# Kernel tuning notes

Hardware: AMD Instinct MI355X
Metric: run time of the kernel (lower is better)

## Reference

```python
import jax, jax.numpy as jnp
import numpy as np

B, D_IN, H1, H2, LAT, K = 32768, 512, 256, 128, 64, 2048
BN_EPS = 1e-5
COMMIT = 0.25


def _linear_w(k, i, o):
    # xavier-uniform-ish init
    lim = np.sqrt(6.0 / (i + o)).astype(np.float32)
    return jax.random.uniform(k, (i, o), jnp.float32, -lim, lim)


def _bn_params(keys, n):
    g = jax.random.uniform(keys[0], (n,), jnp.float32, 0.5, 1.5)
    b = 0.1 * jax.random.normal(keys[1], (n,), jnp.float32)
    m = 0.1 * jax.random.normal(keys[2], (n,), jnp.float32)
    v = jax.random.uniform(keys[3], (n,), jnp.float32, 0.5, 1.5)
    return g, b, m, v


def setup_inputs() -> dict:
    key = jax.random.key(0)
    ks = jax.random.split(key, 32)
    inp = {"x": jax.random.normal(ks[0], (B, D_IN), jnp.float32)}
    # encoder: 512 -> 256 -> 128 -> 64
    inp["ew1"], inp["eb1"] = _linear_w(ks[1], D_IN, H1), jnp.zeros((H1,), jnp.float32)
    inp["eg1"], inp["ebt1"], inp["em1"], inp["ev1"] = _bn_params(jax.random.split(ks[2], 4), H1)
    inp["ew2"], inp["eb2"] = _linear_w(ks[3], H1, H2), jnp.zeros((H2,), jnp.float32)
    inp["eg2"], inp["ebt2"], inp["em2"], inp["ev2"] = _bn_params(jax.random.split(ks[4], 4), H2)
    inp["ew3"], inp["eb3"] = _linear_w(ks[5], H2, LAT), jnp.zeros((LAT,), jnp.float32)
    # codebook (num_embeddings, latent_dim)
    inp["codebook"] = _linear_w(ks[6], K, LAT).reshape(K, LAT)
    # decoder: 64 -> 128 -> 256 -> 512
    inp["dw1"], inp["db1"] = _linear_w(ks[7], LAT, H2), jnp.zeros((H2,), jnp.float32)
    inp["dg1"], inp["dbt1"], inp["dm1"], inp["dv1"] = _bn_params(jax.random.split(ks[8], 4), H2)
    inp["dw2"], inp["db2"] = _linear_w(ks[9], H2, H1), jnp.zeros((H1,), jnp.float32)
    inp["dg2"], inp["dbt2"], inp["dm2"], inp["dv2"] = _bn_params(jax.random.split(ks[10], 4), H1)
    inp["dw3"], inp["db3"] = _linear_w(ks[11], H1, D_IN), jnp.zeros((D_IN,), jnp.float32)
    return inp


def _bn(x, g, b, m, v):
    # BatchNorm1d in eval mode: running stats
    return (x - m) * (g * jax.lax.rsqrt(v + BN_EPS)) + b


def reference(x, ew1, eb1, eg1, ebt1, em1, ev1,
              ew2, eb2, eg2, ebt2, em2, ev2,
              ew3, eb3, codebook,
              dw1, db1, dg1, dbt1, dm1, dv1,
              dw2, db2, dg2, dbt2, dm2, dv2,
              dw3, db3):
    # ---- encoder MLP (Dropout is identity in eval) ----
    h = _bn(jax.nn.relu(x @ ew1 + eb1), eg1, ebt1, em1, ev1)
    h = _bn(jax.nn.relu(h @ ew2 + eb2), eg2, ebt2, em2, ev2)
    z_e = h @ ew3 + eb3  # [B, LAT]

    # ---- vector quantization: cdist + argmin + gather ----
    # squared L2 distance (argmin-equivalent to cdist p=2)
    d2 = (jnp.sum(z_e * z_e, axis=1, keepdims=True)
          + jnp.sum(codebook * codebook, axis=1)[None, :]
          - 2.0 * (z_e @ codebook.T))  # [B, K]
    idx = jnp.argmin(d2, axis=-1)  # [B]
    z_q = codebook[idx]  # gather, [B, LAT]

    codebook_loss = jnp.mean((z_q - jax.lax.stop_gradient(z_e)) ** 2)
    commit_loss = jnp.mean((z_e - jax.lax.stop_gradient(z_q)) ** 2)
    vq_loss = codebook_loss + COMMIT * commit_loss

    # straight-through estimator
    z_q = z_e + jax.lax.stop_gradient(z_q - z_e)

    # ---- decoder MLP ----
    h = _bn(jax.nn.relu(z_q @ dw1 + db1), dg1, dbt1, dm1, dv1)
    h = _bn(jax.nn.relu(h @ dw2 + db2), dg2, dbt2, dm2, dv2)
    x_recon = h @ dw3 + db3  # [B, D_IN]

    recon_err = jnp.mean((x_recon - x) ** 2)
    return x_recon, vq_loss, idx, recon_err
```

## Files before the change

### kernel.cpp

```cpp
#include <hip/hip_runtime.h>

#define B_ROWS 32768
#define D_IN   512
#define H1_N   256
#define H2_N   128
#define LAT_N  64
#define K_CB   2048

#define VQ_MARGIN 6.0e-3f
#define BK 32
#define BN 128

typedef __attribute__((ext_vector_type(8))) short s8v;
typedef __attribute__((ext_vector_type(4))) float f4v;

__device__ inline unsigned short f2bf(float f) {
    union { float f; unsigned u; } v; v.f = f;
    unsigned r = v.u + 0x7fffu + ((v.u >> 16) & 1u);
    return (unsigned short)(r >> 16);
}
__device__ inline float bf2f(unsigned short h) {
    union { unsigned u; float f; } v; v.u = ((unsigned)h) << 16;
    return v.f;
}

__device__ inline int pidx(int r, int k, int K) {
    return ((r >> 4) * (K >> 5) + (k >> 5)) * 512 + (((k >> 3) & 3) << 7)
         + ((r & 15) << 3) + (k & 7);
}

#define SWZ(row) ((((row) >> 2) & 7) << 3)

__global__ __launch_bounds__(256) void xsplit(
    const float* __restrict__ x, unsigned short* __restrict__ xhi,
    unsigned short* __restrict__ xlo)
{
    int t = blockIdx.x * 256 + threadIdx.x;
    int r = t >> 6;
    int g = t & 63;
    const float* p = &x[(size_t)r * D_IN + g * 8];
    float4 v0 = *reinterpret_cast<const float4*>(p);
    float4 v1 = *reinterpret_cast<const float4*>(p + 4);
    float fv[8] = {v0.x, v0.y, v0.z, v0.w, v1.x, v1.y, v1.z, v1.w};
    union { unsigned short s[8]; uint4 v; } H, L;
#pragma unroll
    for (int j = 0; j < 8; ++j) {
        unsigned u = __float_as_uint(fv[j]);
        float lo = fv[j] - __uint_as_float(u & 0xffff0000u);
        H.s[j] = (unsigned short)(u >> 16);
        L.s[j] = f2bf(lo);
    }
    int pp = pidx(r, g * 8, D_IN);
    *reinterpret_cast<uint4*>(&xhi[pp]) = H.v;
    *reinterpret_cast<uint4*>(&xlo[pp]) = L.v;
}

template <int MODE, int K, int CT>
__global__ __launch_bounds__(256, 2) void mfma_gemm(
    const unsigned short* __restrict__ A_hi,
    const unsigned short* __restrict__ A_lo,
    const unsigned short* __restrict__ w_hi,
    const unsigned short* __restrict__ w_lo,
    const float* __restrict__ bias,
    const float* __restrict__ bn_g, const float* __restrict__ bn_b,
    const float* __restrict__ bn_m, const float* __restrict__ bn_v,
    unsigned short* __restrict__ out_hi, unsigned short* __restrict__ out_lo,
    float* __restrict__ out_f32,
    const float* __restrict__ xref, float* __restrict__ partials, int N)
{
    constexpr int NK = K / 32;
    const int lane = threadIdx.x & 63;
    const int wv = threadIdx.x >> 6;
    const int wr = wv >> 1, wc = wv & 1;
    const int rbase = blockIdx.x * 128 + wr * 64;
    const int cbase = blockIdx.y * (32 * CT) + wc * (16 * CT);
    const int lr = lane & 15, lg = lane >> 4;
    const int lofs = lg * 128 + lr * 8;

    f4v acc[4][CT];
#pragma unroll
    for (int rt = 0; rt < 4; ++rt)
#pragma unroll
        for (int ct = 0; ct < CT; ++ct)
            acc[rt][ct] = (f4v){0.f, 0.f, 0.f, 0.f};

    s8v ahA[4], alA[4], bhA[CT], blA[CT];
    s8v ahB[4], alB[4], bhB[CT], blB[CT];

#define LOADF(S, KS)                                                          \
    {                                                                         \
        _Pragma("unroll")                                                     \
        for (int rt = 0; rt < 4; ++rt) {                                      \
            int aoff = (((rbase >> 4) + rt) * NK + (KS)) * 512 + lofs;        \
            ah##S[rt] = *reinterpret_cast<const s8v*>(&A_hi[aoff]);           \
            al##S[rt] = *reinterpret_cast<const s8v*>(&A_lo[aoff]);           \
        }                                                                     \
        _Pragma("unroll")                                                     \
        for (int ct = 0; ct < CT; ++ct) {                                     \
            int woff = (((cbase >> 4) + ct) * NK + (KS)) * 512 + lofs;        \
            bh##S[ct] = *reinterpret_cast<const s8v*>(&w_hi[woff]);           \
            bl##S[ct] = *reinterpret_cast<const s8v*>(&w_lo[woff]);           \
        }                                                                     \
    }

#define MFMAF(S)                                                              \
    {                                                                         \
        _Pragma("unroll")                                                     \
        for (int rt = 0; rt < 4; ++rt)                                        \
            _Pragma("unroll")                                                 \
            for (int ct = 0; ct < CT; ++ct) {                                 \
                acc[rt][ct] = __builtin_amdgcn_mfma_f32_16x16x32_bf16(        \
                    ah##S[rt], bh##S[ct], acc[rt][ct], 0, 0, 0);              \
                acc[rt][ct] = __builtin_amdgcn_mfma_f32_16x16x32_bf16(        \
                    al##S[rt], bh##S[ct], acc[rt][ct], 0, 0, 0);              \
                acc[rt][ct] = __builtin_amdgcn_mfma_f32_16x16x32_bf16(        \
                    ah##S[rt], bl##S[ct], acc[rt][ct], 0, 0, 0);              \
            }                                                                 \
    }

    LOADF(A, 0);
#pragma unroll
    for (int k2 = 0; k2 < NK / 2; ++k2) {
        LOADF(B, 2 * k2 + 1);
        MFMAF(A);
        if (k2 + 1 < NK / 2) LOADF(A, 2 * k2 + 2);
        MFMAF(B);
    }
#undef LOADF
#undef MFMAF

    float sq = 0.f;
#pragma unroll
    for (int ct = 0; ct < CT; ++ct) {
        int col = cbase + ct * 16 + lr;
        float bi = bias[col];
        float sc = 0.f, sh = 0.f;
        if (MODE == 0) {
            float s = bn_g[col] * rsqrtf(bn_v[col] + 1e-5f);
            sc = s;
            sh = bn_b[col] - bn_m[col] * s;
        }
#pragma unroll
        for (int rt = 0; rt < 4; ++rt)
#pragma unroll
            for (int i = 0; i < 4; ++i) {
                int row = rbase + rt * 16 + lg * 4 + i;
                float v = acc[rt][ct][i] + bi;
                if (MODE == 0) v = fmaxf(v, 0.f) * sc + sh;
                if (MODE == 0 || MODE == 3) {
                    unsigned u = __float_as_uint(v);
                    int p = pidx(row, col, N);
                    out_hi[p] = (unsigned short)(u >> 16);
                    out_lo[p] = f2bf(v - __uint_as_float(u & 0xffff0000u));
                }
                if (MODE == 2) {
                    float d = v - xref[(size_t)row * N + col];
                    sq = fmaf(d, d, sq);
                }
                if (MODE == 2 || MODE == 3)
                    out_f32[(size_t)row * N + col] = v;
            }
    }
    if (MODE == 2) {
        __shared__ float red[256];
        red[threadIdx.x] = sq;
        __syncthreads();
        for (int off = 128; off > 0; off >>= 1) {
            if (threadIdx.x < off) red[threadIdx.x] += red[threadIdx.x + off];
            __syncthreads();
        }
        if (threadIdx.x == 0)
            partials[blockIdx.y * gridDim.x + blockIdx.x] = red[0];
    }
}

template <int MODE, bool GATHER>
__global__ __launch_bounds__(256, 6) void rgemm(
    const int* __restrict__ rcnt, const int* __restrict__ rlist,
    const float* __restrict__ A, const float* __restrict__ W,
    const float* __restrict__ bias,
    const float* __restrict__ bn_g, const float* __restrict__ bn_b,
    const float* __restrict__ bn_m, const float* __restrict__ bn_v,
    float* __restrict__ out, int M, int N)
{
    const int count = min(rcnt[0], B_ROWS);
    const int row0 = blockIdx.x * 64;
    if (row0 >= count) return;
    __shared__ float sA[BK][64];
    __shared__ float sB[BK][BN];
    const int tid = threadIdx.x;
    const int tr = tid >> 4;
    const int tc = tid & 15;
    const int n0 = blockIdx.y * BN;

    float acc[4][8];
#pragma unroll
    for (int i = 0; i < 4; ++i)
#pragma unroll
        for (int j = 0; j < 8; ++j) acc[i][j] = 0.f;

    for (int k0 = 0; k0 < M; k0 += BK) {
#pragma unroll
        for (int it = 0; it < 2; ++it) {
            int s = tid + it * 256;
            int m = s >> 3;
            int kq = s & 7;
            int i = row0 + m;
            int src;
            if (GATHER) {
                int rr = (i < count) ? rlist[i] : 0;
                src = ((unsigned)rr < (unsigned)B_ROWS) ? rr : 0;
            } else {
                src = i;
            }
            float4 v = *reinterpret_cast<const float4*>(
                &A[(size_t)src * M + k0 + kq * 4]);
            int kk = kq * 4;
            sA[kk + 0][m ^ SWZ(kk + 0)] = v.x;
            sA[kk + 1][m ^ SWZ(kk + 1)] = v.y;
            sA[kk + 2][m ^ SWZ(kk + 2)] = v.z;
            sA[kk + 3][m ^ SWZ(kk + 3)] = v.w;
        }
#pragma unroll
        for (int it = 0; it < 4; ++it) {
            int s = tid + it * 256;
            int k = s >> 5;
            int nq = s & 31;
            int n = n0 + nq * 4;
            float4 v = make_float4(0.f, 0.f, 0.f, 0.f);
            if (n < N)
                v = *reinterpret_cast<const float4*>(&W[(size_t)(k0 + k) * N + n]);
            *reinterpret_cast<float4*>(&sB[k][nq * 4]) = v;
        }
        __syncthreads();
#pragma unroll 4
        for (int k = 0; k < BK; ++k) {
            int ac = (tr * 4) ^ SWZ(k);
            float4 a0 = *reinterpret_cast<float4*>(&sA[k][ac]);
            float a[4] = {a0.x, a0.y, a0.z, a0.w};
            float4 b0 = *reinterpret_cast<float4*>(&sB[k][tc * 4]);
            float4 b1 = *reinterpret_cast<float4*>(&sB[k][64 + tc * 4]);
            float b[8] = {b0.x, b0.y, b0.z, b0.w, b1.x, b1.y, b1.z, b1.w};
#pragma unroll
            for (int i = 0; i < 4; ++i)
#pragma unroll
                for (int j = 0; j < 8; ++j)
                    acc[i][j] = fmaf(a[i], b[j], acc[i][j]);
        }
        __syncthreads();
    }

    const int nb0 = n0 + tc * 4;
    const int nb1 = n0 + 64 + tc * 4;
    float bi[8], sc[8], sh[8];
#pragma unroll
    for (int g = 0; g < 2; ++g) {
        int nb = g ? nb1 : nb0;
        if (nb < N) {
#pragma unroll
            for (int j = 0; j < 4; ++j) {
                int n = nb + j;
                bi[g * 4 + j] = bias[n];
                if (MODE == 0) {
                    float s = bn_g[n] * rsqrtf(bn_v[n] + 1e-5f);
                    sc[g * 4 + j] = s;
                    sh[g * 4 + j] = bn_b[n] - bn_m[n] * s;
                }
            }
        }
    }
#pragma unroll
    for (int i = 0; i < 4; ++i) {
        int row = row0 + tr * 4 + i;
#pragma unroll
        for (int g = 0; g < 2; ++g) {
            int nb = g ? nb1 : nb0;
            if (nb < N) {
                float o[4];
#pragma unroll
                for (int j = 0; j < 4; ++j) {
                    float v = acc[i][g * 4 + j] + bi[g * 4 + j];
                    if (MODE == 0) {
                        v = v > 0.f ? v : 0.f;
                        v = v * sc[g * 4 + j] + sh[g * 4 + j];
                    }
                    o[j] = v;
                }
                *reinterpret_cast<float4*>(&out[(size_t)row * N + nb]) =
                    make_float4(o[0], o[1], o[2], o[3]);
            }
        }
    }
}

__device__ inline void wprep_packed(const float* __restrict__ w,
                                    unsigned short* __restrict__ w_hi,
                                    unsigned short* __restrict__ w_lo,
                                    int K, int N, int t)
{
    if (t >= N * (K >> 3)) return;
    int n = t / (K >> 3);
    int k0 = (t - n * (K >> 3)) << 3;
    union { unsigned short s[8]; uint4 v; } H, L;
#pragma unroll
    for (int j = 0; j < 8; ++j) {
        float f = w[(size_t)(k0 + j) * N + n];
        unsigned u = __float_as_uint(f);
        float lo = f - __uint_as_float(u & 0xffff0000u);
        H.s[j] = (unsigned short)(u >> 16);
        L.s[j] = f2bf(lo);
    }
    int p = pidx(n, k0, K);
    *reinterpret_cast<uint4*>(&w_hi[p]) = H.v;
    *reinterpret_cast<uint4*>(&w_lo[p]) = L.v;
}

__global__ __launch_bounds__(256) void prep_all(
    const float* __restrict__ dw3, unsigned short* w3hi, unsigned short* w3lo,
    const float* __restrict__ dw2, unsigned short* w2hi, unsigned short* w2lo,
    const float* __restrict__ dw1, unsigned short* w1hi, unsigned short* w1lo,
    const float* __restrict__ ew1, unsigned short* e1hi, unsigned short* e1lo,
    const float* __restrict__ ew2, unsigned short* e2hi, unsigned short* e2lo,
    const float* __restrict__ ew3, unsigned short* e3hi, unsigned short* e3lo,
    const float* __restrict__ cb, unsigned short* cb_hi, unsigned short* cb_lo,
    float* __restrict__ cn, int* __restrict__ rcnt, float* __restrict__ repairp)
{
    int bid = blockIdx.x;
    int tid = threadIdx.x;
    if (bid < 64) {
        wprep_packed(dw3, w3hi, w3lo, H1_N, D_IN, bid * 256 + tid);
    } else if (bid < 80) {
        wprep_packed(dw2, w2hi, w2lo, H2_N, H1_N, (bid - 64) * 256 + tid);
    } else if (bid < 84) {
        wprep_packed(dw1, w1hi, w1lo, LAT_N, H2_N, (bid - 80) * 256 + tid);
    } else if (bid < 148) {
        wprep_packed(ew1, e1hi, e1lo, D_IN, H1_N, (bid - 84) * 256 + tid);
    } else if (bid < 164) {
        wprep_packed(ew2, e2hi, e2lo, H1_N, H2_N, (bid - 148) * 256 + tid);
    } else if (bid < 168) {
        wprep_packed(ew3, e3hi, e3lo, H2_N, LAT_N, (bid - 164) * 256 + tid);
    } else {
        int blk = bid - 168;
        if (blk == 0) {
            if (tid == 0) rcnt[0] = 0;
            repairp[tid] = 0.f;
        }
        int j = blk * 256 + tid;
        float s = 0.f;
#pragma unroll
        for (int g = 0; g < 8; ++g) {
            float4 v0 = *reinterpret_cast<const float4*>(&cb[(size_t)j * LAT_N + g * 8]);
            float4 v1 = *reinterpret_cast<const float4*>(&cb[(size_t)j * LAT_N + g * 8 + 4]);
            float e[8] = {v0.x, v0.y, v0.z, v0.w, v1.x, v1.y, v1.z, v1.w};
            union { unsigned short us[8]; uint4 v; } H, L;
#pragma unroll
            for (int t = 0; t < 8; ++t) {
                s = fmaf(e[t], e[t], s);
                unsigned short hb = f2bf(e[t]);
                H.us[t] = hb;
                L.us[t] = f2bf(e[t] - bf2f(hb));
            }
            int p = pidx(j, g * 8, LAT_N);
            *reinterpret_cast<uint4*>(&cb_hi[p]) = H.v;
            *reinterpret_cast<uint4*>(&cb_lo[p]) = L.v;
        }
        cn[j] = s;
    }
}

__global__ __launch_bounds__(256) void vq_mfma(
    const unsigned short* __restrict__ zhi, const unsigned short* __restrict__ zlo,
    const unsigned short* __restrict__ cb_hi,
    const unsigned short* __restrict__ cb_lo, const float* __restrict__ cnorm,
    float4* __restrict__ cand)
{
    const int lane = threadIdx.x & 63;
    const int wid  = blockIdx.x * 4 + (threadIdx.x >> 6);
    const int rbase = (wid >> 3) * 64;
    const int cblk  = wid & 7;
    const int cbase = cblk * 256;
    const int lr = lane & 15;
    const int lg = lane >> 4;

    s8v a_hi[4][2], a_lo[4][2];
#pragma unroll
    for (int rt = 0; rt < 4; ++rt) {
#pragma unroll
        for (int ks = 0; ks < 2; ++ks) {
            int off = (((rbase >> 4) + rt) * 2 + ks) * 512 + lg * 128 + lr * 8;
            a_hi[rt][ks] = *reinterpret_cast<const s8v*>(&zhi[off]);
            a_lo[rt][ks] = *reinterpret_cast<const s8v*>(&zlo[off]);
        }
    }

    float b1[4][4], b2[4][4];
    int j1[4][4];
#pragma unroll
    for (int rt = 0; rt < 4; ++rt)
#pragma unroll
        for (int i = 0; i < 4; ++i) {
            b1[rt][i] = 3.4e38f; b2[rt][i] = 3.4e38f; j1[rt][i] = 0;
        }

    for (int ct = 0; ct < 16; ++ct) {
        int col = cbase + ct * 16 + lr;
        int t0 = (((cbase >> 4) + ct) * 2 + 0) * 512 + lg * 128 + lr * 8;
        int t1 = t0 + 512;
        s8v bh0 = *reinterpret_cast<const s8v*>(&cb_hi[t0]);
        s8v bh1 = *reinterpret_cast<const s8v*>(&cb_hi[t1]);
        s8v bl0 = *reinterpret_cast<const s8v*>(&cb_lo[t0]);
        s8v bl1 = *reinterpret_cast<const s8v*>(&cb_lo[t1]);
        float cn = cnorm[col];
#pragma unroll
        for (int rt = 0; rt < 4; ++rt) {
            f4v acc = {0.f, 0.f, 0.f, 0.f};
            acc = __builtin_amdgcn_mfma_f32_16x16x32_bf16(a_hi[rt][0], bh0, acc, 0, 0, 0);
            acc = __builtin_amdgcn_mfma_f32_16x16x32_bf16(a_hi[rt][1], bh1, acc, 0, 0, 0);
            acc = __builtin_amdgcn_mfma_f32_16x16x32_bf16(a_lo[rt][0], bh0, acc, 0, 0, 0);
            acc = __builtin_amdgcn_mfma_f32_16x16x32_bf16(a_lo[rt][1], bh1, acc, 0, 0, 0);
            acc = __builtin_amdgcn_mfma_f32_16x16x32_bf16(a_hi[rt][0], bl0, acc, 0, 0, 0);
            acc = __builtin_amdgcn_mfma_f32_16x16x32_bf16(a_hi[rt][1], bl1, acc, 0, 0, 0);
#pragma unroll
            for (int i = 0; i < 4; ++i) {
                float d = fmaf(-2.f, acc[i], cn);
                if (d < b1[rt][i]) {
                    b2[rt][i] = b1[rt][i];
                    b1[rt][i] = d;
                    j1[rt][i] = col;
                } else if (d < b2[rt][i]) {
                    b2[rt][i] = d;
                }
            }
        }
    }

#pragma unroll
    for (int off = 1; off < 16; off <<= 1) {
#pragma unroll
        for (int rt = 0; rt < 4; ++rt)
#pragma unroll
            for (int i = 0; i < 4; ++i) {
                float o1 = __shfl_xor(b1[rt][i], off);
                float o2 = __shfl_xor(b2[rt][i], off);
                int oj = __shfl_xor(j1[rt][i], off);
                float nb2 = fminf(fmaxf(b1[rt][i], o1), fminf(b2[rt][i], o2));
                if (o1 < b1[rt][i] ||
                    (o1 == b1[rt][i] && oj < j1[rt][i])) {
                    b1[rt][i] = o1;
                    j1[rt][i] = oj;
                }
                b2[rt][i] = nb2;
            }
    }
    if (lr == 0) {
#pragma unroll
        for (int rt = 0; rt < 4; ++rt)
#pragma unroll
            for (int i = 0; i < 4; ++i) {
                int row = rbase + rt * 16 + lg * 4 + i;
                cand[(size_t)row * 8 + cblk] = make_float4(
                    b1[rt][i], __int_as_float(j1[rt][i]), b2[rt][i], 0.f);
            }
    }
}

__global__ __launch_bounds__(256) void vq_merge(
    const float4* __restrict__ cand, const float* __restrict__ z,
    const float* __restrict__ cb,
    const unsigned short* __restrict__ cbhi,
    const unsigned short* __restrict__ cblo,
    unsigned short* __restrict__ zqhi, unsigned short* __restrict__ zqlo,
    float* __restrict__ idxf,
    int* __restrict__ rlist, int* __restrict__ rcnt,
    float* __restrict__ mergep)
{
    __shared__ float red[256];
    int tid = threadIdx.x;
    int row = blockIdx.x * 256 + tid;
    const float4* c = &cand[(size_t)row * 8];
    float4 c0 = c[0];
    float b1 = c0.x, b2 = c0.z;
    int j1 = __float_as_int(c0.y);
#pragma unroll
    for (int t = 1; t < 8; ++t) {
        float4 ct = c[t];
        float o1 = ct.x, o2 = ct.z;
        int oj = __float_as_int(ct.y);
        float nb2 = fminf(fmaxf(b1, o1), fminf(b2, o2));
        if (o1 < b1 || (o1 == b1 && oj < j1)) { b1 = o1; j1 = oj; }
        b2 = nb2;
    }
    idxf[row] = (float)j1;
    float sq = 0.f;
    if (b2 - b1 >= VQ_MARGIN) {
#pragma unroll
        for (int lq = 0; lq < 16; ++lq) {
            float4 cv = *reinterpret_cast<const float4*>(&cb[(size_t)j1 * LAT_N + lq * 4]);
            float4 zv = *reinterpret_cast<const float4*>(&z[(size_t)row * LAT_N + lq * 4]);
            float d0 = cv.x - zv.x, d1 = cv.y - zv.y;
            float d2 = cv.z - zv.z, d3 = cv.w - zv.w;
            sq = fmaf(d0, d0, sq); sq = fmaf(d1, d1, sq);
            sq = fmaf(d2, d2, sq); sq = fmaf(d3, d3, sq);
        }
#pragma unroll
        for (int g = 0; g < 8; ++g) {
            int sp = pidx(j1, g * 8, LAT_N);
            int dp = pidx(row, g * 8, LAT_N);
            *reinterpret_cast<uint4*>(&zqhi[dp]) =
                *reinterpret_cast<const uint4*>(&cbhi[sp]);
            *reinterpret_cast<uint4*>(&zqlo[dp]) =
                *reinterpret_cast<const uint4*>(&cblo[sp]);
        }
    } else {
        int s = atomicAdd(rcnt, 1);
        if (s < B_ROWS) rlist[s] = row;
    }
    red[tid] = sq;
    __syncthreads();
    for (int off = 128; off > 0; off >>= 1) {
        if (tid < off) red[tid] += red[tid + off];
        __syncthreads();
    }
    if (tid == 0) mergep[blockIdx.x] = red[0];
}

#define RB 8
__global__ __launch_bounds__(256) void repair_scan(
    const int* __restrict__ rcnt, const int* __restrict__ rlist,
    const float* __restrict__ zr,
    const float* __restrict__ cb, const float* __restrict__ cn,
    const unsigned short* __restrict__ cbhi,
    const unsigned short* __restrict__ cblo,
    unsigned short* __restrict__ zqhi, unsigned short* __restrict__ zqlo,
    float* __restrict__ idxf, float* __restrict__ repairp)
{
    __shared__ float sz[RB][LAT_N];
    __shared__ float rv[256];
    __shared__ int ri[256];
    const int tid = threadIdx.x;
    const int count = min(rcnt[0], B_ROWS);
    if (blockIdx.x * RB >= count) return;
    float lsum = 0.f;
    for (int base = blockIdx.x * RB; base < count; base += gridDim.x * RB) {
        int nr = min(RB, count - base);
        __syncthreads();
        for (int s = tid; s < nr * LAT_N; s += 256) {
            int r = s >> 6, d = s & 63;
            sz[r][d] = zr[(size_t)(base + r) * LAT_N + d];
        }
        __syncthreads();
        float bv[RB];
        int bj[RB];
#pragma unroll
        for (int r = 0; r < RB; ++r) { bv[r] = 3.4e38f; bj[r] = 0; }
        for (int k = 0; k < K_CB / 256; ++k) {
            int cidx = tid + k * 256;
            float a[RB];
#pragma unroll
            for (int r = 0; r < RB; ++r) a[r] = 0.f;
            const float* cp = &cb[(size_t)cidx * LAT_N];
#pragma unroll 2
            for (int d4 = 0; d4 < 16; ++d4) {
                float4 cv = *reinterpret_cast<const float4*>(cp + d4 * 4);
#pragma unroll
                for (int r = 0; r < RB; ++r) {
                    a[r] = fmaf(sz[r][d4 * 4 + 0], cv.x, a[r]);
                    a[r] = fmaf(sz[r][d4 * 4 + 1], cv.y, a[r]);
                    a[r] = fmaf(sz[r][d4 * 4 + 2], cv.z, a[r]);
                    a[r] = fmaf(sz[r][d4 * 4 + 3], cv.w, a[r]);
                }
            }
            float cnv = cn[cidx];
#pragma unroll
            for (int r = 0; r < RB; ++r) {
                float d = fmaf(-2.f, a[r], cnv);
                if (d < bv[r] || (d == bv[r] && cidx < bj[r])) {
                    bv[r] = d; bj[r] = cidx;
                }
            }
        }
        for (int r = 0; r < RB; ++r) {
            if (r >= nr) break;
            rv[tid] = bv[r];
            ri[tid] = bj[r];
            __syncthreads();
            for (int off = 128; off > 0; off >>= 1) {
                if (tid < off) {
                    float ov = rv[tid + off];
                    int oi = ri[tid + off];
                    if (ov < rv[tid] || (ov == rv[tid] && oi < ri[tid])) {
                        rv[tid] = ov; ri[tid] = oi;
                    }
                }
                __syncthreads();
            }
            int bjf = ri[0];
            int rr = rlist[base + r];
            bool ok = (unsigned)rr < (unsigned)B_ROWS;
            rr = ok ? rr : 0;
            if (tid == 0 && ok) idxf[rr] = (float)bjf;
            float v = 0.f;
            if (tid < 64) {
                float d = cb[(size_t)bjf * LAT_N + tid] - sz[r][tid];
                v = d * d;
            }
            __syncthreads();
            rv[tid] = v;
            __syncthreads();
            for (int off = 128; off > 0; off >>= 1) {
                if (tid < off) rv[tid] += rv[tid + off];
                __syncthreads();
            }
            if (tid == 0) lsum += rv[0];
            if (ok) {
                if (tid < 8) {
                    int g = tid;
                    *reinterpret_cast<uint4*>(&zqhi[pidx(rr, g * 8, LAT_N)]) =
                        *reinterpret_cast<const uint4*>(&cbhi[pidx(bjf, g * 8, LAT_N)]);
                } else if (tid < 16) {
                    int g = tid - 8;
                    *reinterpret_cast<uint4*>(&zqlo[pidx(rr, g * 8, LAT_N)]) =
                        *reinterpret_cast<const uint4*>(&cblo[pidx(bjf, g * 8, LAT_N)]);
                }
            }
            __syncthreads();
        }
    }
    if (tid == 0) repairp[blockIdx.x] = lsum;
}

__global__ __launch_bounds__(256) void finalize_kernel(
    const float* __restrict__ mergep, int nm,
    const float* __restrict__ repairp, int nr,
    const float* __restrict__ rep, int nre,
    float* __restrict__ vq_out, float* __restrict__ re_out)
{
    __shared__ float s[256];
    int tid = threadIdx.x;
    float a = 0.f;
    for (int i = tid; i < nm; i += 256) a += mergep[i];
    for (int i = tid; i < nr; i += 256) a += repairp[i];
    s[tid] = a;
    __syncthreads();
    for (int off = 128; off > 0; off >>= 1) {
        if (tid < off) s[tid] += s[tid + off];
        __syncthreads();
    }
    if (tid == 0) *vq_out = 1.25f * s[0] / (float)(B_ROWS * LAT_N);
    __syncthreads();
    float b = 0.f;
    for (int i = tid; i < nre; i += 256) b += rep[i];
    s[tid] = b;
    __syncthreads();
    for (int off = 128; off > 0; off >>= 1) {
        if (tid < off) s[tid] += s[tid + off];
        __syncthreads();
    }
    if (tid == 0) *re_out = s[0] / (float)(B_ROWS * D_IN);
}

extern "C" void kernel_launch(void* const* d_in, const int* in_sizes, int n_in,
                              void* d_out, int out_size, void* d_ws, size_t ws_size,
                              hipStream_t stream)
{
    const float* x    = (const float*)d_in[0];
    const float* ew1  = (const float*)d_in[1];
    const float* eb1  = (const float*)d_in[2];
    const float* eg1  = (const float*)d_in[3];
    const float* ebt1 = (const float*)d_in[4];
    const float* em1  = (const float*)d_in[5];
    const float* ev1  = (const float*)d_in[6];
    const float* ew2  = (const float*)d_in[7];
    const float* eb2  = (const float*)d_in[8];
    const float* eg2  = (const float*)d_in[9];
    const float* ebt2 = (const float*)d_in[10];
    const float* em2  = (const float*)d_in[11];
    const float* ev2  = (const float*)d_in[12];
    const float* ew3  = (const float*)d_in[13];
    const float* eb3  = (const float*)d_in[14];
    const float* cb   = (const float*)d_in[15];
    const float* dw1  = (const float*)d_in[16];
    const float* db1  = (const float*)d_in[17];
    const float* dg1  = (const float*)d_in[18];
    const float* dbt1 = (const float*)d_in[19];
    const float* dm1  = (const float*)d_in[20];
    const float* dv1  = (const float*)d_in[21];
    const float* dw2  = (const float*)d_in[22];
    const float* db2  = (const float*)d_in[23];
    const float* dg2  = (const float*)d_in[24];
    const float* dbt2 = (const float*)d_in[25];
    const float* dm2  = (const float*)d_in[26];
    const float* dv2  = (const float*)d_in[27];
    const float* dw3  = (const float*)d_in[28];
    const float* db3  = (const float*)d_in[29];

    float* outf = (float*)d_out;
    const size_t XR_OFF = 0;
    const size_t VQ_OFF = (size_t)B_ROWS * D_IN;
    const size_t IDX_OFF = VQ_OFF + 1;
    const size_t RE_OFF = IDX_OFF + B_ROWS;

    float* wsf = (float*)d_ws;
    size_t off = 0;
    float* buf256 = wsf + off; off += (size_t)B_ROWS * H1_N;
    float* buf128 = wsf + off; off += (size_t)B_ROWS * H2_N;
    float* zbuf   = wsf + off; off += (size_t)B_ROWS * LAT_N;
    float* zr     = wsf + off; off += (size_t)B_ROWS * LAT_N;
    float* cnbuf  = wsf + off; off += K_CB;
    float* mergep = wsf + off; off += 128;
    float* repairp= wsf + off; off += 256;
    float* rep    = wsf + off; off += 1024;
    unsigned short* cbhi = (unsigned short*)(wsf + off); off += K_CB * LAT_N / 2;
    unsigned short* cblo = (unsigned short*)(wsf + off); off += K_CB * LAT_N / 2;
    float4* candb = (float4*)(wsf + off); off += (size_t)B_ROWS * 8 * 4;
    int* rcnt  = (int*)(wsf + off); off += 16;
    int* rlist = (int*)(wsf + off); off += B_ROWS;
    unsigned short* w1hi = (unsigned short*)(wsf + off); off += (H2_N * LAT_N) / 2;
    unsigned short* w1lo = (unsigned short*)(wsf + off); off += (H2_N * LAT_N) / 2;
    unsigned short* w2hi = (unsigned short*)(wsf + off); off += (H1_N * H2_N) / 2;
    unsigned short* w2lo = (unsigned short*)(wsf + off); off += (H1_N * H2_N) / 2;
    unsigned short* w3hi = (unsigned short*)(wsf + off); off += (D_IN * H1_N) / 2;
    unsigned short* w3lo = (unsigned short*)(wsf + off); off += (D_IN * H1_N) / 2;
    unsigned short* e1hi = (unsigned short*)(wsf + off); off += (D_IN * H1_N) / 2;
    unsigned short* e1lo = (unsigned short*)(wsf + off); off += (D_IN * H1_N) / 2;
    unsigned short* e2hi = (unsigned short*)(wsf + off); off += (H1_N * H2_N) / 2;
    unsigned short* e2lo = (unsigned short*)(wsf + off); off += (H1_N * H2_N) / 2;
    unsigned short* e3hi = (unsigned short*)(wsf + off); off += (H2_N * LAT_N) / 2;
    unsigned short* e3lo = (unsigned short*)(wsf + off); off += (H2_N * LAT_N) / 2;
    unsigned short* zqhi = (unsigned short*)(wsf + off); off += (size_t)B_ROWS * LAT_N / 2;
    unsigned short* zqlo = (unsigned short*)(wsf + off); off += (size_t)B_ROWS * LAT_N / 2;
    unsigned short* xhi  = (unsigned short*)(wsf + off); off += (size_t)B_ROWS * D_IN / 2;
    unsigned short* xlo  = (unsigned short*)(wsf + off); off += (size_t)B_ROWS * D_IN / 2;

    unsigned short* eh1hi = (unsigned short*)buf256;
    unsigned short* eh1lo = (unsigned short*)(buf256 + (size_t)B_ROWS * 128);
    unsigned short* zhi   = (unsigned short*)buf256;
    unsigned short* zlo   = (unsigned short*)(buf256 + (size_t)B_ROWS * 32);
    float*          h1r   = buf256;
    unsigned short* dh2hi = (unsigned short*)buf256;
    unsigned short* dh2lo = (unsigned short*)(buf256 + (size_t)B_ROWS * 128);
    unsigned short* eh2hi = (unsigned short*)buf128;
    unsigned short* eh2lo = (unsigned short*)(buf128 + (size_t)B_ROWS * 64);
    float*          h2r   = buf128;
    unsigned short* dh1hi = (unsigned short*)buf128;
    unsigned short* dh1lo = (unsigned short*)(buf128 + (size_t)B_ROWS * 64);

    dim3 blk(256);
    const int GXM = B_ROWS / 128;
    const int GM64 = B_ROWS / 64;

    prep_all<<<dim3(176), blk, 0, stream>>>(
        dw3, w3hi, w3lo, dw2, w2hi, w2lo, dw1, w1hi, w1lo,
        ew1, e1hi, e1lo, ew2, e2hi, e2lo, ew3, e3hi, e3lo,
        cb, cbhi, cblo, cnbuf, rcnt, repairp);
    xsplit<<<dim3(B_ROWS * (D_IN / 8) / 256), blk, 0, stream>>>(x, xhi, xlo);

    mfma_gemm<0, D_IN, 4><<<dim3(GXM, H1_N / 128), blk, 0, stream>>>(
        xhi, xlo, e1hi, e1lo, eb1, eg1, ebt1, em1, ev1,
        eh1hi, eh1lo, nullptr, nullptr, nullptr, H1_N);
    mfma_gemm<0, H1_N, 4><<<dim3(GXM, 1), blk, 0, stream>>>(
        eh1hi, eh1lo, e2hi, e2lo, eb2, eg2, ebt2, em2, ev2,
        eh2hi, eh2lo, nullptr, nullptr, nullptr, H2_N);
    mfma_gemm<3, H2_N, 2><<<dim3(GXM, 1), blk, 0, stream>>>(
        eh2hi, eh2lo, e3hi, e3lo, eb3, nullptr, nullptr, nullptr, nullptr,
        zhi, zlo, zbuf, nullptr, nullptr, LAT_N);

    vq_mfma<<<dim3(1024), blk, 0, stream>>>(zhi, zlo, cbhi, cblo, cnbuf, candb);
    vq_merge<<<dim3(B_ROWS / 256), blk, 0, stream>>>(
        candb, zbuf, cb, cbhi, cblo, zqhi, zqlo,
        outf + IDX_OFF, rlist, rcnt, mergep);

    rgemm<0, true><<<dim3(GM64, 2), blk, 0, stream>>>(
        rcnt, rlist, x, ew1, eb1, eg1, ebt1, em1, ev1, h1r, D_IN, H1_N);
    rgemm<0, false><<<dim3(GM64, 1), blk, 0, stream>>>(
        rcnt, rlist, h1r, ew2, eb2, eg2, ebt2, em2, ev2, h2r, H1_N, H2_N);
    rgemm<1, false><<<dim3(GM64, 1), blk, 0, stream>>>(
        rcnt, rlist, h2r, ew3, eb3, nullptr, nullptr, nullptr, nullptr,
        zr, H2_N, LAT_N);
    repair_scan<<<dim3(256), blk, 0, stream>>>(
        rcnt, rlist, zr, cb, cnbuf, cbhi, cblo, zqhi, zqlo,
        outf + IDX_OFF, repairp);

    mfma_gemm<0, LAT_N, 4><<<dim3(GXM, 1), blk, 0, stream>>>(
        zqhi, zqlo, w1hi, w1lo, db1, dg1, dbt1, dm1, dv1,
        dh1hi, dh1lo, nullptr, nullptr, nullptr, H2_N);
    mfma_gemm<0, H2_N, 4><<<dim3(GXM, H1_N / 128), blk, 0, stream>>>(
        dh1hi, dh1lo, w2hi, w2lo, db2, dg2, dbt2, dm2, dv2,
        dh2hi, dh2lo, nullptr, nullptr, nullptr, H1_N);
    mfma_gemm<2, H1_N, 4><<<dim3(GXM, D_IN / 128), blk, 0, stream>>>(
        dh2hi, dh2lo, w3hi, w3lo, db3, nullptr, nullptr, nullptr, nullptr,
        nullptr, nullptr, outf + XR_OFF, x, rep, D_IN);

    finalize_kernel<<<dim3(1), blk, 0, stream>>>(
        mergep, 128, repairp, 256, rep, 1024, outf + VQ_OFF, outf + RE_OFF);
}
```

Before: 470.4 us.

## Stage A tiles through LDS via direct global-to-LDS loads in MLP GEMM

The MLP GEMM kernel now copies the activation hi/lo tiles into a double-buffered LDS array using global_load_lds, so the two column-warps share one copy instead of each fetching the same A fragments from global memory. Weight fragments are still loaded per warp from global memory, and a __syncthreads is added on every k-step. Launch bounds are raised to 3 blocks per CU to improve occupancy. In exchange it adds barriers and LDS use, drops the previous register double-buffering of weights, and may raise register pressure or introduce synchronisation stalls.

```diff
diff --git a/kernel.cpp b/kernel.cpp
--- a/kernel.cpp
+++ b/kernel.cpp
@@ -27,6 +27,12 @@
 __device__ inline int pidx(int r, int k, int K) {
     return ((r >> 4) * (K >> 5) + (k >> 5)) * 512 + (((k >> 3) & 3) << 7)
          + ((r & 15) << 3) + (k & 7);
+}
+
+__device__ inline void gload_lds16(const unsigned short* g, unsigned short* l) {
+    __builtin_amdgcn_global_load_lds(
+        (const __attribute__((address_space(1))) unsigned int*)g,
+        (__attribute__((address_space(3))) unsigned int*)l, 16, 0, 0);
 }
 
 #define SWZ(row) ((((row) >> 2) & 7) << 3)
@@ -56,7 +62,7 @@
 }
 
 template <int MODE, int K, int CT>
-__global__ __launch_bounds__(256, 2) void mfma_gemm(
+__global__ __launch_bounds__(256, 3) void mfma_gemm(
     const unsigned short* __restrict__ A_hi,
     const unsigned short* __restrict__ A_lo,
     const unsigned short* __restrict__ w_hi,
@@ -69,10 +75,12 @@
     const float* __restrict__ xref, float* __restrict__ partials, int N)
 {
     constexpr int NK = K / 32;
+    __shared__ __align__(16) unsigned short ldsA[2][2][8][512];
     const int lane = threadIdx.x & 63;
     const int wv = threadIdx.x >> 6;
     const int wr = wv >> 1, wc = wv & 1;
     const int rbase = blockIdx.x * 128 + wr * 64;
+    const int rtile0 = blockIdx.x * 8;
     const int cbase = blockIdx.y * (32 * CT) + wc * (16 * CT);
     const int lr = lane & 15, lg = lane >> 4;
     const int lofs = lg * 128 + lr * 8;
@@ -84,50 +92,55 @@
         for (int ct = 0; ct < CT; ++ct)
             acc[rt][ct] = (f4v){0.f, 0.f, 0.f, 0.f};
 
-    s8v ahA[4], alA[4], bhA[CT], blA[CT];
-    s8v ahB[4], alB[4], bhB[CT], blB[CT];
-
-#define LOADF(S, KS)                                                          \
+#define STAGE(BUF, KS)                                                        \
     {                                                                         \
         _Pragma("unroll")                                                     \
-        for (int rt = 0; rt < 4; ++rt) {                                      \
-            int aoff = (((rbase >> 4) + rt) * NK + (KS)) * 512 + lofs;        \
-            ah##S[rt] = *reinterpret_cast<const s8v*>(&A_hi[aoff]);           \
-            al##S[rt] = *reinterpret_cast<const s8v*>(&A_lo[aoff]);           \
+        for (int p = 0; p < 4; ++p) {                                         \
+            int piece = wv * 4 + p;                                \
+            int hl = piece >> 3, tile = piece & 7;                            \
+            const unsigned short* src =                                       \
+                (hl ? A_lo : A_hi) + ((rtile0 + tile) * NK + (KS)) * 512 +    \
+                lane * 8;                                                     \
+            gload_lds16(src, &ldsA[BUF][hl][tile][0]);                        \
         }                                                                     \
-        _Pragma("unroll")                                                     \
-        for (int ct = 0; ct < CT; ++ct) {                                     \
-            int woff = (((cbase >> 4) + ct) * NK + (KS)) * 512 + lofs;        \
-            bh##S[ct] = *reinterpret_cast<const s8v*>(&w_hi[woff]);           \
-            bl##S[ct] = *reinterpret_cast<const s8v*>(&w_lo[woff]);           \
-        }                                                                     \
-    }
-
-#define MFMAF(S)                                                              \
-    {                                                                         \
-        _Pragma("unroll")                                                     \
-        for (int rt = 0; rt < 4; ++rt)                                        \
-            _Pragma("unroll")                                                 \
-            for (int ct = 0; ct < CT; ++ct) {                                 \
-                acc[rt][ct] = __builtin_amdgcn_mfma_f32_16x16x32_bf16(        \
-                    ah##S[rt], bh##S[ct], acc[rt][ct], 0, 0, 0);              \
-                acc[rt][ct] = __builtin_amdgcn_mfma_f32_16x16x32_bf16(        \
-                    al##S[rt], bh##S[ct], acc[rt][ct], 0, 0, 0);              \
-                acc[rt][ct] = __builtin_amdgcn_mfma_f32_16x16x32_bf16(        \
-                    ah##S[rt], bl##S[ct], acc[rt][ct], 0, 0, 0);              \
-            }                                                                 \
-    }
-
-    LOADF(A, 0);
-#pragma unroll
-    for (int k2 = 0; k2 < NK / 2; ++k2) {
-        LOADF(B, 2 * k2 + 1);
-        MFMAF(A);
-        if (k2 + 1 < NK / 2) LOADF(A, 2 * k2 + 2);
-        MFMAF(B);
-    }
-#undef LOADF
-#undef MFMAF
+    }
+
+    STAGE(0, 0);
+    __syncthreads();
+    int cur = 0;
+#pragma unroll
+    for (int ks = 0; ks < NK; ++ks) {
+        if (ks + 1 < NK) STAGE(cur ^ 1, ks + 1);
+        s8v bh[CT], bl[CT];
+#pragma unroll
+        for (int ct = 0; ct < CT; ++ct) {
+            int woff = (((cbase >> 4) + ct) * NK + ks) * 512 + lofs;
+            bh[ct] = *reinterpret_cast<const s8v*>(&w_hi[woff]);
+            bl[ct] = *reinterpret_cast<const s8v*>(&w_lo[woff]);
+        }
+        s8v ah[4], al[4];
+#pragma unroll
+        for (int rt = 0; rt < 4; ++rt) {
+            ah[rt] = *reinterpret_cast<const s8v*>(
+                &ldsA[cur][0][wr * 4 + rt][lofs]);
+            al[rt] = *reinterpret_cast<const s8v*>(
+                &ldsA[cur][1][wr * 4 + rt][lofs]);
+        }
+#pragma unroll
+        for (int rt = 0; rt < 4; ++rt)
+#pragma unroll
+            for (int ct = 0; ct < CT; ++ct) {
+                acc[rt][ct] = __builtin_amdgcn_mfma_f32_16x16x32_bf16(
+                    ah[rt], bh[ct], acc[rt][ct], 0, 0, 0);
+                acc[rt][ct] = __builtin_amdgcn_mfma_f32_16x16x32_bf16(
+                    al[rt], bh[ct], acc[rt][ct], 0, 0, 0);
+                acc[rt][ct] = __builtin_amdgcn_mfma_f32_16x16x32_bf16(
+                    ah[rt], bl[ct], acc[rt][ct], 0, 0, 0);
+            }
+        __syncthreads();
+        cur ^= 1;
+    }
+#undef STAGE
 
     float sq = 0.f;
 #pragma unroll
```

Result: faster. 452.5 us (-3.8%).
